# Kernel tuning notes

Measured on AMD Instinct MI355X. Metric: run time of the kernel, lower is better.

The kernel has to match this reference:

```python
import jax, jax.numpy as jnp
import numpy as np

N_NODES = 100000
N_EDGES = 640000
F = 128          # in_features
MID = 192        # (2*F + OUT)//2
OUT = 128


def setup_inputs() -> dict:
    key = jax.random.key(0)
    k_h, k_dr, k_s, k_d, k_w1, k_w2 = jax.random.split(key, 6)
    h = jax.random.normal(k_h, (N_NODES, F), dtype=jnp.float32)
    dR = jax.random.uniform(k_dr, (N_EDGES,), dtype=jnp.float32)
    src_idx = jax.random.randint(k_s, (N_EDGES,), 0, N_NODES)
    dst_idx = jax.random.randint(k_d, (N_EDGES,), 0, N_NODES)
    W1 = jax.random.normal(k_w1, (2 * F + 1, MID), dtype=jnp.float32) * (1.0 / np.sqrt(2 * F + 1))
    b1 = jnp.zeros((MID,), dtype=jnp.float32)
    W2 = jax.random.normal(k_w2, (MID, OUT), dtype=jnp.float32) * (1.0 / np.sqrt(MID))
    b2 = jnp.zeros((OUT,), dtype=jnp.float32)
    return {"h": h, "dR": dR, "src_idx": src_idx, "dst_idx": dst_idx,
            "W1": W1, "b1": b1, "W2": W2, "b2": b2}


def reference(h, dR, src_idx, dst_idx, W1, b1, W2, b2):
    # first=True branch: cat([dst_hidden, src_hidden, dR[:, None]]) -> [E, 2F+1]
    inp = jnp.concatenate([h[dst_idx], h[src_idx], dR[:, None]], axis=1)
    hid = jax.nn.relu(inp @ W1 + b1)          # [E, MID]
    out = jnp.tanh(hid @ W2 + b2)             # [E, OUT]
    return out
```

## Files before the change

### kernel.cpp

```cpp
#include <hip/hip_runtime.h>


#define F_IN   128
#define MID    192
#define OUT_N  128
#define K1     256
#define M_TILE 64
#define H_STRIDE 200
#define NBLK   512

typedef __attribute__((ext_vector_type(8))) short bf16x8;
typedef __attribute__((ext_vector_type(8))) unsigned short u16x8;
typedef __attribute__((ext_vector_type(4))) float f32x4;

__device__ __forceinline__ unsigned short f2bf(float f) {
    unsigned u = __builtin_bit_cast(unsigned, f);
    u = (u + 0x7FFFu + ((u >> 16) & 1u)) >> 16;
    return (unsigned short)u;
}

__global__ void pack_weights(const float* __restrict__ W1,
                             const float* __restrict__ W2,
                             unsigned short* __restrict__ p1,
                             unsigned short* __restrict__ p2,
                             float* __restrict__ wdr) {
    int i = blockIdx.x * 256 + threadIdx.x;
    if (i < K1 * MID) {
        int kin = i & 31;
        int rest = i >> 5;
        int n = rest % MID;
        int kt = rest / MID;
        p1[i] = f2bf(W1[(kt * 32 + kin) * MID + n]);
    }
    int j = i - K1 * MID;
    if (j >= 0 && j < MID * OUT_N) {
        int kin = j & 31;
        int rest = j >> 5;
        int n = rest & 127;
        int kt = rest >> 7;
        p2[j] = f2bf(W2[(kt * 32 + kin) * OUT_N + n]);
    }
    if (i < MID) wdr[i] = W1[256 * MID + i];
}

__global__ void hconv(const float* __restrict__ h,
                      unsigned short* __restrict__ hb, int n8) {
    int i = blockIdx.x * 256 + threadIdx.x;
    if (i >= n8) return;
    const float4* hp = (const float4*)h;
    float4 v0 = hp[2 * i];
    float4 v1 = hp[2 * i + 1];
    u16x8 o;
    o[0] = f2bf(v0.x); o[1] = f2bf(v0.y); o[2] = f2bf(v0.z); o[3] = f2bf(v0.w);
    o[4] = f2bf(v1.x); o[5] = f2bf(v1.y); o[6] = f2bf(v1.z); o[7] = f2bf(v1.w);
    *((u16x8*)hb + i) = o;
}

#define SBAR()  do { __builtin_amdgcn_sched_barrier(0); \
                     __builtin_amdgcn_s_barrier();      \
                     __builtin_amdgcn_sched_barrier(0); } while (0)

__global__ __launch_bounds__(256, 2)
void edge_mlp_kernel(const unsigned short* __restrict__ hb,
                     const float* __restrict__ dR,
                     const int*   __restrict__ src_idx,
                     const int*   __restrict__ dst_idx,
                     const float* __restrict__ b1,
                     const float* __restrict__ b2,
                     const unsigned short* __restrict__ p1,
                     const unsigned short* __restrict__ p2,
                     const float* __restrict__ wdr,
                     float* __restrict__ out,
                     int NT) {
    __shared__ __align__(16) unsigned short sA[2][M_TILE * 256];

    const int tid  = threadIdx.x;
    const int lane = tid & 63;
    const int w    = tid >> 6;
    const int l15  = lane & 15;
    const int q    = lane >> 4;

    const int g    = lane >> 4;
    const int c    = lane & 15;
    const int part = g & 1;
    const int* __restrict__ ip = part ? src_idx : dst_idx;
    const int eb   = w * 16 + (g >> 1);

    bf16x8 w1f[8][3];
#pragma unroll
    for (int kt = 0; kt < 8; ++kt)
#pragma unroll
        for (int ni = 0; ni < 3; ++ni) {
            const int nb = (w + ni * 4) * 16 + l15;
            w1f[kt][ni] = *(const bf16x8*)(&p1[((kt * MID + nb) << 5) + (q << 3)]);
        }
    bf16x8 w2f[6][2];
#pragma unroll
    for (int kt = 0; kt < 6; ++kt)
#pragma unroll
        for (int ni = 0; ni < 2; ++ni) {
            const int nb = (w + ni * 4) * 16 + l15;
            w2f[kt][ni] = *(const bf16x8*)(&p2[((kt * OUT_N + nb) << 5) + (q << 3)]);
        }
    float bb1[3], wd1[3], bb2[2];
#pragma unroll
    for (int ni = 0; ni < 3; ++ni) {
        const int n = (w + ni * 4) * 16 + l15;
        bb1[ni] = b1[n]; wd1[ni] = wdr[n];
    }
#pragma unroll
    for (int ni = 0; ni < 2; ++ni) bb2[ni] = b2[(w + ni * 4) * 16 + l15];

    const int t0 = blockIdx.x;
    if (t0 >= NT) return;

    int idxc[8];
    {
        const int base = t0 * M_TILE + eb;
#pragma unroll
        for (int i = 0; i < 8; ++i) idxc[i] = ip[base + 2 * i];
#pragma unroll
        for (int i = 0; i < 8; ++i) {
            const int el = eb + 2 * i;
            const unsigned short* gp =
                hb + ((size_t)idxc[i] << 7) + ((c ^ (el & 7)) << 3);
            unsigned short* lp = &sA[0][(w * 16 + 2 * i) * 256];
            __builtin_amdgcn_global_load_lds(
                (const __attribute__((address_space(1))) void*)gp,
                (__attribute__((address_space(3))) void*)lp, 16, 0, 0);
        }
    }
    int t1 = t0 + NBLK; if (t1 > NT - 1) t1 = NT - 1;
    {
        const int base = t1 * M_TILE + eb;
#pragma unroll
        for (int i = 0; i < 8; ++i) idxc[i] = ip[base + 2 * i];
    }
    float dr_now = dR[t0 * M_TILE + lane];
    float dr_nxt = dR[t1 * M_TILE + lane];

    int cur = 0;
    for (int t = t0; t < NT; t += NBLK, cur ^= 1) {
#pragma unroll
        for (int i = 0; i < 8; ++i) {
            const int el = eb + 2 * i;
            const unsigned short* gp =
                hb + ((size_t)idxc[i] << 7) + ((c ^ (el & 7)) << 3);
            unsigned short* lp = &sA[cur ^ 1][(w * 16 + 2 * i) * 256];
            __builtin_amdgcn_global_load_lds(
                (const __attribute__((address_space(1))) void*)gp,
                (__attribute__((address_space(3))) void*)lp, 16, 0, 0);
        }
        {
            int t2 = t + 2 * NBLK; if (t2 > NT - 1) t2 = NT - 1;
            const int base = t2 * M_TILE + eb;
#pragma unroll
            for (int i = 0; i < 8; ++i) idxc[i] = ip[base + 2 * i];
        }
        SBAR();

        const unsigned short* sAc = &sA[cur][0];
        f32x4 acc1[4][3] = {};
#pragma unroll
        for (int kt = 0; kt < 8; ++kt) {
            bf16x8 a[4];
#pragma unroll
            for (int m = 0; m < 4; ++m) {
                const int r = m * 16 + l15;
                a[m] = *(const bf16x8*)(&sAc[r * 256 + (((kt * 4 + q) ^ (r & 7)) << 3)]);
            }
#pragma unroll
            for (int ni = 0; ni < 3; ++ni)
#pragma unroll
                for (int m = 0; m < 4; ++m)
                    acc1[m][ni] = __builtin_amdgcn_mfma_f32_16x16x32_bf16(
                        a[m], w1f[kt][ni], acc1[m][ni], 0, 0, 0);
        }
        SBAR();

        float drv[16];
#pragma unroll
        for (int m = 0; m < 4; ++m)
#pragma unroll
            for (int r = 0; r < 4; ++r)
                drv[m * 4 + r] = __shfl(dr_now, m * 16 + q * 4 + r);

        unsigned short* sH = &sA[cur][0];
#pragma unroll
        for (int ni = 0; ni < 3; ++ni) {
            const int n = (w + ni * 4) * 16 + l15;
#pragma unroll
            for (int m = 0; m < 4; ++m)
#pragma unroll
                for (int r = 0; r < 4; ++r) {
                    const int e = m * 16 + q * 4 + r;
                    float v = acc1[m][ni][r] + bb1[ni] + drv[m * 4 + r] * wd1[ni];
                    v = fmaxf(v, 0.0f);
                    sH[e * H_STRIDE + n] = f2bf(v);
                }
        }
        asm volatile("s_waitcnt lgkmcnt(0)" ::: "memory");
        SBAR();

        f32x4 acc2[4][2] = {};
#pragma unroll
        for (int kt = 0; kt < 6; ++kt) {
            bf16x8 a[4];
#pragma unroll
            for (int m = 0; m < 4; ++m)
                a[m] = *(const bf16x8*)(&sH[(m * 16 + l15) * H_STRIDE + kt * 32 + q * 8]);
#pragma unroll
            for (int ni = 0; ni < 2; ++ni)
#pragma unroll
                for (int m = 0; m < 4; ++m)
                    acc2[m][ni] = __builtin_amdgcn_mfma_f32_16x16x32_bf16(
                        a[m], w2f[kt][ni], acc2[m][ni], 0, 0, 0);
        }
        SBAR();

#pragma unroll
        for (int ni = 0; ni < 2; ++ni) {
            const int n = (w + ni * 4) * 16 + l15;
#pragma unroll
            for (int m = 0; m < 4; ++m)
#pragma unroll
                for (int r = 0; r < 4; ++r) {
                    const int e = t * M_TILE + m * 16 + q * 4 + r;
                    float x = acc2[m][ni][r] + bb2[ni];
                    x = fminf(fmaxf(x, -10.0f), 10.0f);
                    float tt = __expf(2.0f * x);
                    out[(size_t)e * OUT_N + n] = (tt - 1.0f) * __builtin_amdgcn_rcpf(tt + 1.0f);
                }
        }

        dr_now = dr_nxt;
        {
            int t2 = t + 2 * NBLK; if (t2 > NT - 1) t2 = NT - 1;
            dr_nxt = dR[t2 * M_TILE + lane];
        }
    }
}

extern "C" void kernel_launch(void* const* d_in, const int* in_sizes, int n_in,
                              void* d_out, int out_size, void* d_ws, size_t ws_size,
                              hipStream_t stream) {
    const float* h   = (const float*)d_in[0];
    const float* dR  = (const float*)d_in[1];
    const int* src   = (const int*)d_in[2];
    const int* dst   = (const int*)d_in[3];
    const float* W1  = (const float*)d_in[4];
    const float* b1  = (const float*)d_in[5];
    const float* W2  = (const float*)d_in[6];
    const float* b2  = (const float*)d_in[7];
    float* out       = (float*)d_out;

    const int hn = in_sizes[0];
    const int E  = in_sizes[1];
    const int NT = E / M_TILE;

    unsigned short* hbuf = (unsigned short*)d_ws;
    unsigned short* p1   = hbuf + hn;
    unsigned short* p2   = p1 + K1 * MID;
    float* wdr           = (float*)(p2 + MID * OUT_N);

    hconv<<<(hn / 8 + 255) / 256, 256, 0, stream>>>(h, hbuf, hn / 8);
    pack_weights<<<(K1 * MID + MID * OUT_N + 255) / 256, 256, 0, stream>>>(W1, W2, p1, p2, wdr);

    const int grid = NT < NBLK ? NT : NBLK;
    edge_mlp_kernel<<<grid, 256, 0, stream>>>(hbuf, dR, src, dst, b1, b2, p1, p2, wdr, out, NT);
}
```

Baseline: 503.4 us.

## Transpose MFMA operands, stream W1 per k-step, and vectorize LDS/output stores

Swaps the MFMA operand order so weights are the A operand and edge rows the B operand, which makes each lane's four accumulator values contiguous along the feature dimension. This allows packed 8-byte bf16 stores into the hidden tile and 16-byte nontemporal float4 stores to the output in place of scalar stores. W1 fragments are no longer kept resident in registers. They are reloaded from global/L2 on every k-step, cutting register pressure at the cost of extra memory traffic per tile. Biases are now loaded as vectors inside the loop.

```diff
diff --git a/kernel.cpp b/kernel.cpp
--- a/kernel.cpp
+++ b/kernel.cpp
@@ -12,6 +12,7 @@
 typedef __attribute__((ext_vector_type(8))) short bf16x8;
 typedef __attribute__((ext_vector_type(8))) unsigned short u16x8;
 typedef __attribute__((ext_vector_type(4))) float f32x4;
+typedef __attribute__((ext_vector_type(2))) unsigned int u32x2;
 
 __device__ __forceinline__ unsigned short f2bf(float f) {
     unsigned u = __builtin_bit_cast(unsigned, f);
@@ -86,30 +87,14 @@
     const int* __restrict__ ip = part ? src_idx : dst_idx;
     const int eb   = w * 16 + (g >> 1);
 
-    bf16x8 w1f[8][3];
-#pragma unroll
-    for (int kt = 0; kt < 8; ++kt)
-#pragma unroll
-        for (int ni = 0; ni < 3; ++ni) {
-            const int nb = (w + ni * 4) * 16 + l15;
-            w1f[kt][ni] = *(const bf16x8*)(&p1[((kt * MID + nb) << 5) + (q << 3)]);
-        }
     bf16x8 w2f[6][2];
 #pragma unroll
     for (int kt = 0; kt < 6; ++kt)
 #pragma unroll
-        for (int ni = 0; ni < 2; ++ni) {
-            const int nb = (w + ni * 4) * 16 + l15;
-            w2f[kt][ni] = *(const bf16x8*)(&p2[((kt * OUT_N + nb) << 5) + (q << 3)]);
-        }
-    float bb1[3], wd1[3], bb2[2];
-#pragma unroll
-    for (int ni = 0; ni < 3; ++ni) {
-        const int n = (w + ni * 4) * 16 + l15;
-        bb1[ni] = b1[n]; wd1[ni] = wdr[n];
-    }
-#pragma unroll
-    for (int ni = 0; ni < 2; ++ni) bb2[ni] = b2[(w + ni * 4) * 16 + l15];
+        for (int mi = 0; mi < 2; ++mi) {
+            const int nb = (2 * w + mi) * 16 + l15;
+            w2f[kt][mi] = *(const bf16x8*)(&p2[((kt * OUT_N + nb) << 5) + (q << 3)]);
+        }
 
     const int t0 = blockIdx.x;
     if (t0 >= NT) return;
@@ -160,77 +145,93 @@
         SBAR();
 
         const unsigned short* sAc = &sA[cur][0];
-        f32x4 acc1[4][3] = {};
-#pragma unroll
+        f32x4 acc1[3][4] = {};
         for (int kt = 0; kt < 8; ++kt) {
-            bf16x8 a[4];
-#pragma unroll
-            for (int m = 0; m < 4; ++m) {
-                const int r = m * 16 + l15;
-                a[m] = *(const bf16x8*)(&sAc[r * 256 + (((kt * 4 + q) ^ (r & 7)) << 3)]);
-            }
-#pragma unroll
-            for (int ni = 0; ni < 3; ++ni)
-#pragma unroll
-                for (int m = 0; m < 4; ++m)
-                    acc1[m][ni] = __builtin_amdgcn_mfma_f32_16x16x32_bf16(
-                        a[m], w1f[kt][ni], acc1[m][ni], 0, 0, 0);
-        }
-        SBAR();
-
-        float drv[16];
-#pragma unroll
-        for (int m = 0; m < 4; ++m)
-#pragma unroll
-            for (int r = 0; r < 4; ++r)
-                drv[m * 4 + r] = __shfl(dr_now, m * 16 + q * 4 + r);
+            bf16x8 bfr[4];
+#pragma unroll
+            for (int et = 0; et < 4; ++et) {
+                const int r = et * 16 + l15;
+                bfr[et] = *(const bf16x8*)(&sAc[r * 256 + (((kt * 4 + q) ^ (r & 7)) << 3)]);
+            }
+            bf16x8 w1a[3];
+#pragma unroll
+            for (int mi = 0; mi < 3; ++mi) {
+                const int nb = (3 * w + mi) * 16 + l15;
+                w1a[mi] = *(const bf16x8*)(&p1[((kt * MID + nb) << 5) + (q << 3)]);
+            }
+#pragma unroll
+            for (int mi = 0; mi < 3; ++mi)
+#pragma unroll
+                for (int et = 0; et < 4; ++et)
+                    acc1[mi][et] = __builtin_amdgcn_mfma_f32_16x16x32_bf16(
+                        w1a[mi], bfr[et], acc1[mi][et], 0, 0, 0);
+        }
+        SBAR();
+
+        float drl[4];
+#pragma unroll
+        for (int et = 0; et < 4; ++et) drl[et] = __shfl(dr_now, et * 16 + l15);
 
         unsigned short* sH = &sA[cur][0];
 #pragma unroll
-        for (int ni = 0; ni < 3; ++ni) {
-            const int n = (w + ni * 4) * 16 + l15;
-#pragma unroll
-            for (int m = 0; m < 4; ++m)
+        for (int mi = 0; mi < 3; ++mi) {
+            const int n0 = (3 * w + mi) * 16 + q * 4;
+            const f32x4 bb = *(const f32x4*)(b1 + n0);
+            const f32x4 wd = *(const f32x4*)(wdr + n0);
+#pragma unroll
+            for (int et = 0; et < 4; ++et) {
+                const int e = et * 16 + l15;
+                unsigned pk0, pk1;
+                {
+                    float v0 = fmaxf(acc1[mi][et][0] + bb[0] + drl[et] * wd[0], 0.0f);
+                    float v1 = fmaxf(acc1[mi][et][1] + bb[1] + drl[et] * wd[1], 0.0f);
+                    float v2 = fmaxf(acc1[mi][et][2] + bb[2] + drl[et] * wd[2], 0.0f);
+                    float v3 = fmaxf(acc1[mi][et][3] + bb[3] + drl[et] * wd[3], 0.0f);
+                    pk0 = (unsigned)f2bf(v0) | ((unsigned)f2bf(v1) << 16);
+                    pk1 = (unsigned)f2bf(v2) | ((unsigned)f2bf(v3) << 16);
+                }
+                u32x2 pk; pk[0] = pk0; pk[1] = pk1;
+                *(u32x2*)(&sH[e * H_STRIDE + n0]) = pk;
+            }
+        }
+        asm volatile("s_waitcnt lgkmcnt(0)" ::: "memory");
+        SBAR();
+
+        f32x4 acc2[2][4] = {};
+        for (int kt = 0; kt < 6; ++kt) {
+            bf16x8 hfr[4];
+#pragma unroll
+            for (int et = 0; et < 4; ++et)
+                hfr[et] = *(const bf16x8*)(&sH[(et * 16 + l15) * H_STRIDE + kt * 32 + q * 8]);
+#pragma unroll
+            for (int mi = 0; mi < 2; ++mi)
+#pragma unroll
+                for (int et = 0; et < 4; ++et)
+                    acc2[mi][et] = __builtin_amdgcn_mfma_f32_16x16x32_bf16(
+                        w2f[kt][mi], hfr[et], acc2[mi][et], 0, 0, 0);
+        }
+        SBAR();
+
+        f32x4 bb2v[2];
+#pragma unroll
+        for (int mi = 0; mi < 2; ++mi)
+            bb2v[mi] = *(const f32x4*)(b2 + (2 * w + mi) * 16 + q * 4);
+#pragma unroll
+        for (int et = 0; et < 4; ++et) {
+            const size_t e = (size_t)(t * M_TILE + et * 16 + l15);
+#pragma unroll
+            for (int mi = 0; mi < 2; ++mi) {
+                const int n0 = (2 * w + mi) * 16 + q * 4;
+                f32x4 y;
 #pragma unroll
                 for (int r = 0; r < 4; ++r) {
-                    const int e = m * 16 + q * 4 + r;
-                    float v = acc1[m][ni][r] + bb1[ni] + drv[m * 4 + r] * wd1[ni];
-                    v = fmaxf(v, 0.0f);
-                    sH[e * H_STRIDE + n] = f2bf(v);
-                }
-        }
-        asm volatile("s_waitcnt lgkmcnt(0)" ::: "memory");
-        SBAR();
-
-        f32x4 acc2[4][2] = {};
-#pragma unroll
-        for (int kt = 0; kt < 6; ++kt) {
-            bf16x8 a[4];
-#pragma unroll
-            for (int m = 0; m < 4; ++m)
-                a[m] = *(const bf16x8*)(&sH[(m * 16 + l15) * H_STRIDE + kt * 32 + q * 8]);
-#pragma unroll
-            for (int ni = 0; ni < 2; ++ni)
-#pragma unroll
-                for (int m = 0; m < 4; ++m)
-                    acc2[m][ni] = __builtin_amdgcn_mfma_f32_16x16x32_bf16(
-                        a[m], w2f[kt][ni], acc2[m][ni], 0, 0, 0);
-        }
-        SBAR();
-
-#pragma unroll
-        for (int ni = 0; ni < 2; ++ni) {
-            const int n = (w + ni * 4) * 16 + l15;
-#pragma unroll
-            for (int m = 0; m < 4; ++m)
-#pragma unroll
-                for (int r = 0; r < 4; ++r) {
-                    const int e = t * M_TILE + m * 16 + q * 4 + r;
-                    float x = acc2[m][ni][r] + bb2[ni];
+                    float x = acc2[mi][et][r] + bb2v[mi][r];
                     x = fminf(fmaxf(x, -10.0f), 10.0f);
                     float tt = __expf(2.0f * x);
-                    out[(size_t)e * OUT_N + n] = (tt - 1.0f) * __builtin_amdgcn_rcpf(tt + 1.0f);
+                    y[r] = (tt - 1.0f) * __builtin_amdgcn_rcpf(tt + 1.0f);
                 }
+                __builtin_nontemporal_store(y, (f32x4*)(out + e * OUT_N + n0));
+            }
         }
 
         dr_now = dr_nxt;
```

Result: slower. 566.8 us (+12.6%).
